# Optimization experiments

Hardware: AMD Instinct MI355X
Metric: run time of the kernel (lower is better)

Reference implementation:

```python
import jax, jax.numpy as jnp
import numpy as np

N_NODES = 100000

def gcn_conv(x, W, b, src, dst, n):
    # PyG GCNConv: h = x @ W; add self-loops; norm = D^-1/2 (A+I) D^-1/2; aggregate at dst.
    h = x @ W  # [N, out]
    deg = jnp.zeros((n,), h.dtype).at[dst].add(1.0) + 1.0  # +1 for self-loop
    d = jax.lax.rsqrt(deg)  # deg >= 1 always
    norm = d[src] * d[dst]  # [E]
    agg = jnp.zeros_like(h).at[dst].add(norm[:, None] * h[src])  # scatter-add neighbor messages
    agg = agg + h * (d * d)[:, None]  # self-loop contribution (norm = d_i^2)
    return agg + b


def setup_inputs() -> dict:
    key = jax.random.key(0)
    k1, k2, k3, k4 = jax.random.split(key, 4)
    F_in, H, C = 128, 64, 16
    E = 3200000
    x = jax.random.normal(k1, (N_NODES, F_in), dtype=jnp.float32)
    edges = jax.random.randint(k2, (E, 2), 0, N_NODES, dtype=jnp.int64)
    # Glorot-style init for weights, zero bias (as in GCNConv.reset_parameters)
    W1 = jax.random.normal(k3, (F_in, H), dtype=jnp.float32) * (1.0 / np.sqrt(F_in))
    b1 = jnp.zeros((H,), jnp.float32)
    W2 = jax.random.normal(k4, (H, C), dtype=jnp.float32) * (1.0 / np.sqrt(H))
    b2 = jnp.zeros((C,), jnp.float32)
    return {"x": x, "edges": edges, "W1": W1, "b1": b1, "W2": W2, "b2": b2}


def reference(x, edges, W1, b1, W2, b2):
    src, dst = edges[:, 0], edges[:, 1]
    h = jax.nn.relu(gcn_conv(x, W1, b1, src, dst, N_NODES))
    out = gcn_conv(h, W2, b2, src, dst, N_NODES)
    return out
```

## Files before the change

### kernel.cpp

```cpp
#include <hip/hip_runtime.h>

#define N_NODES 100000
#define F_IN    128
#define H_DIM   64
#define C_DIM   16
#define NBKT    391
#define CHUNK   8192
#define CAP     8960
#define MAXCH   400

typedef __attribute__((ext_vector_type(8))) short bf16x8;
typedef __attribute__((ext_vector_type(4))) float f32x4;

__device__ __forceinline__ unsigned bfr(float f) {
    unsigned u = __float_as_uint(f);
    return (u + (((u >> 16) & 1u) + 0x7FFFu)) >> 16;
}
__device__ __forceinline__ void accb(float4& a, uint2 u) {
    a.x += __uint_as_float(u.x << 16);
    a.y += __uint_as_float(u.x & 0xFFFF0000u);
    a.z += __uint_as_float(u.y << 16);
    a.w += __uint_as_float(u.y & 0xFFFF0000u);
}

__global__ __launch_bounds__(512) void k_bfill(const int2* __restrict__ edges,
                                               int* __restrict__ pairs_flat,
                                               int* __restrict__ cnts_g,
                                               int* __restrict__ lbase_g, int E) {
    __shared__ int2 sp[CHUNK];
    __shared__ int  cnt[NBKT];
    __shared__ int  lbase[NBKT];
    __shared__ int  scn[512];
    int t = threadIdx.x;
    for (int i = t; i < NBKT; i += 512) cnt[i] = 0;
    __syncthreads();
    int base = blockIdx.x * CHUNK;
    int m    = min(E - base, CHUNK);
    int2 ed[16];
    int  rk[16];
    #pragma unroll
    for (int i = 0; i < 16; ++i) {
        int e = i * 512 + t;
        if (e < m) {
            ed[i] = edges[base + e];
            rk[i] = atomicAdd(&cnt[ed[i].y >> 8], 1);
        }
    }
    __syncthreads();
    scn[t] = (t < NBKT) ? cnt[t] : 0;
    __syncthreads();
    #pragma unroll
    for (int off = 1; off < 512; off <<= 1) {
        int v = (t >= off) ? scn[t - off] : 0;
        __syncthreads();
        scn[t] += v;
        __syncthreads();
    }
    for (int b = t; b < NBKT; b += 512) {
        int c = cnt[b];
        int lb = scn[b] - c;
        lbase[b] = lb;
        cnts_g [blockIdx.x * NBKT + b] = c;
        lbase_g[blockIdx.x * NBKT + b] = lb;
    }
    __syncthreads();
    #pragma unroll
    for (int i = 0; i < 16; ++i) {
        int e = i * 512 + t;
        if (e < m) sp[lbase[ed[i].y >> 8] + rk[i]] = ed[i];
    }
    __syncthreads();
    #pragma unroll
    for (int i = 0; i < 16; ++i) {
        int idx = i * 512 + t;
        if (idx < m) {
            int2 p = sp[idx];
            pairs_flat[base + idx] = (p.x << 8) | (p.y & 255);
        }
    }
}

__global__ __launch_bounds__(1024) void k_bnode(const int* __restrict__ pairs_flat,
                                                const int* __restrict__ cnts_g,
                                                const int* __restrict__ lbase_g,
                                                int* __restrict__ csr_src,
                                                int* __restrict__ node_base,
                                                int* __restrict__ node_cnt,
                                                float* __restrict__ dinv, int nch) {
    __shared__ int spairs[CAP];
    __shared__ int sc[CAP];
    __shared__ int rcnt[MAXCH];
    __shared__ int rlb[MAXCH];
    __shared__ int roff[MAXCH];
    __shared__ int scn[512];
    __shared__ int cnt[256];
    __shared__ int row[256];
    __shared__ int wsum[4];
    __shared__ int mtot;
    int b = blockIdx.x;
    int t = threadIdx.x;
    if (t < 256) cnt[t] = 0;
    for (int i = t; i < nch; i += 1024) {
        rcnt[i] = cnts_g [i * NBKT + b];
        rlb[i]  = lbase_g[i * NBKT + b];
    }
    __syncthreads();
    if (t < 512) scn[t] = (t < nch) ? rcnt[t] : 0;
    __syncthreads();
    #pragma unroll
    for (int off = 1; off < 512; off <<= 1) {
        int v = 0;
        if (t < 512 && t >= off) v = scn[t - off];
        __syncthreads();
        if (t < 512) scn[t] += v;
        __syncthreads();
    }
    if (t < nch) roff[t] = scn[t] - rcnt[t];
    if (t == 0) mtot = scn[nch - 1];
    __syncthreads();
    int m = min(mtot, CAP);
    int grp = t >> 4, l16 = t & 15;
    for (int r = grp; r < nch; r += 64) {
        int c  = rcnt[r];
        int ro = roff[r];
        int rb = r * CHUNK + rlb[r];
        for (int j = l16; j < c; j += 16) {
            int pos = ro + j;
            if (pos < CAP) {
                int p  = pairs_flat[rb + j];
                int rk = atomicAdd(&cnt[p & 255], 1);
                spairs[pos] = p | (rk << 25);
            }
        }
    }
    __syncthreads();
    if (t < 256) {
        int c = cnt[t];
        int lane = t & 63, wv = t >> 6;
        int v = c;
        #pragma unroll
        for (int off = 1; off < 64; off <<= 1) {
            int u = __shfl_up(v, off);
            if (lane >= off) v += u;
        }
        if (lane == 63) wsum[wv] = v;
        __syncthreads();
        int woff = 0;
        #pragma unroll
        for (int w = 0; w < 4; ++w) woff += (w < wv) ? wsum[w] : 0;
        int incl = v + woff;
        row[t] = incl - c;
        int node = b * 256 + t;
        if (node < N_NODES) {
            node_base[node] = b * CAP + incl - c;
            node_cnt[node]  = c;
            dinv[node]      = rsqrtf((float)(c + 1));
        }
    } else {
        __syncthreads();
    }
    __syncthreads();
    for (int e = t; e < m; e += 1024) {
        int p = spairs[e];
        sc[row[p & 255] + ((unsigned)p >> 25)] = (p >> 8) & 0x1FFFF;
    }
    __syncthreads();
    for (int e = t; e < m; e += 1024)
        csr_src[b * CAP + e] = sc[e];
}

__global__ __launch_bounds__(256) void k_gemm1(const float* __restrict__ x,
                                               const float* __restrict__ W1,
                                               const float* __restrict__ dinv,
                                               uint2* __restrict__ g1b) {
    __shared__ short wt[64][132];
    int tid = threadIdx.x;
    {
        int n  = tid & 63;
        int k0 = (tid >> 6) * 32;
        #pragma unroll 8
        for (int k = 0; k < 32; ++k)
            wt[n][k0 + k] = (short)bfr(W1[(size_t)(k0 + k) * H_DIM + n]);
    }
    __syncthreads();

    int wave = tid >> 6, lane = tid & 63;
    int tile = blockIdx.x * 4 + wave;
    bool valid = tile < N_NODES / 16;
    int row0 = (valid ? tile : 0) * 16;
    int l15  = lane & 15;
    int kg   = lane >> 4;
    const float* xrow = x + (size_t)(row0 + l15) * F_IN;

    f32x4 ac0 = {0.f,0.f,0.f,0.f}, ac1 = ac0, ac2 = ac0, ac3 = ac0;
    #pragma unroll
    for (int ks = 0; ks < 4; ++ks) {
        int kb = ks * 32 + kg * 8;
        float4 p0 = *(const float4*)(xrow + kb);
        float4 p1 = *(const float4*)(xrow + kb + 4);
        bf16x8 a;
        a[0] = (short)bfr(p0.x); a[1] = (short)bfr(p0.y);
        a[2] = (short)bfr(p0.z); a[3] = (short)bfr(p0.w);
        a[4] = (short)bfr(p1.x); a[5] = (short)bfr(p1.y);
        a[6] = (short)bfr(p1.z); a[7] = (short)bfr(p1.w);
        bf16x8 b0 = *(const bf16x8*)&wt[l15     ][kb];
        bf16x8 b1 = *(const bf16x8*)&wt[l15 + 16][kb];
        bf16x8 b2 = *(const bf16x8*)&wt[l15 + 32][kb];
        bf16x8 b3 = *(const bf16x8*)&wt[l15 + 48][kb];
        ac0 = __builtin_amdgcn_mfma_f32_16x16x32_bf16(a, b0, ac0, 0, 0, 0);
        ac1 = __builtin_amdgcn_mfma_f32_16x16x32_bf16(a, b1, ac1, 0, 0, 0);
        ac2 = __builtin_amdgcn_mfma_f32_16x16x32_bf16(a, b2, ac2, 0, 0, 0);
        ac3 = __builtin_amdgcn_mfma_f32_16x16x32_bf16(a, b3, ac3, 0, 0, 0);
    }
    if (!valid) return;

    int rbase = row0 + kg * 4;
    #pragma unroll
    for (int r = 0; r < 4; ++r) {
        float di = dinv[rbase + r];
        size_t gro = (size_t)(rbase + r) * 16;
        #pragma unroll
        for (int ct = 0; ct < 4; ++ct) {
            float v = ((ct == 0) ? ac0[r] : (ct == 1) ? ac1[r] :
                       (ct == 2) ? ac2[r] : ac3[r]) * di;
            float v1 = __shfl_down(v, 1);
            float v2 = __shfl_down(v, 2);
            float v3 = __shfl_down(v, 3);
            if ((l15 & 3) == 0) {
                uint2 pk;
                pk.x = bfr(v)  | (bfr(v1) << 16);
                pk.y = bfr(v2) | (bfr(v3) << 16);
                g1b[gro + ct * 4 + (l15 >> 2)] = pk;
            }
        }
    }
}

__global__ __launch_bounds__(256) void k_gather1(const int* __restrict__ csr_src,
                                                 const int* __restrict__ base,
                                                 const int* __restrict__ cnt,
                                                 const float* __restrict__ dinv,
                                                 const uint2* __restrict__ g1b,
                                                 const float* __restrict__ b1,
                                                 const float* __restrict__ W2,
                                                 uint2* __restrict__ g2b) {
    __shared__ float  w2t[16 * 68];
    __shared__ float4 ysh[4][68];
    int tid = threadIdx.x;
    #pragma unroll
    for (int i = 0; i < 4; ++i) {
        int idx = i * 256 + tid;
        w2t[(idx & 15) * 68 + (idx >> 4)] = W2[idx];
    }
    __syncthreads();

    int lane = tid & 63;
    int wv   = tid >> 6;
    int grp  = lane >> 4;
    int l16  = lane & 15;
    int g0   = lane & 48;
    int node = ((blockIdx.x * 256 + tid) >> 6) * 4 + grp;
    int   b  = base[node];
    int   c  = cnt[node];
    float di = dinv[node];
    float4 acc = {0.f, 0.f, 0.f, 0.f};
    accb(acc, g1b[(size_t)node * 16 + l16]);

    for (int k0 = 0; k0 < c; k0 += 16) {
        int k = k0 + l16;
        int sidx = (k < c) ? csr_src[b + k] : 0;
        int nj = min(16, c - k0);
        int j = 0;
        for (; j + 4 <= nj; j += 4) {
            int s0 = __shfl(sidx, g0 + j + 0);
            int s1 = __shfl(sidx, g0 + j + 1);
            int s2 = __shfl(sidx, g0 + j + 2);
            int s3 = __shfl(sidx, g0 + j + 3);
            uint2 u0 = g1b[(size_t)s0 * 16 + l16];
            uint2 u1 = g1b[(size_t)s1 * 16 + l16];
            uint2 u2 = g1b[(size_t)s2 * 16 + l16];
            uint2 u3 = g1b[(size_t)s3 * 16 + l16];
            accb(acc, u0); accb(acc, u1); accb(acc, u2); accb(acc, u3);
        }
        for (; j < nj; ++j) {
            accb(acc, g1b[(size_t)__shfl(sidx, g0 + j) * 16 + l16]);
        }
    }

    float4 bv = ((const float4*)b1)[l16];
    float4 y;
    y.x = fmaxf(fmaf(di, acc.x, bv.x), 0.f) * di;
    y.y = fmaxf(fmaf(di, acc.y, bv.y), 0.f) * di;
    y.z = fmaxf(fmaf(di, acc.z, bv.z), 0.f) * di;
    y.w = fmaxf(fmaf(di, acc.w, bv.w), 0.f) * di;
    ysh[wv][grp * 17 + l16] = y;

    float o = 0.f;
    #pragma unroll
    for (int f4 = 0; f4 < 16; ++f4) {
        float4 yv = ysh[wv][grp * 17 + f4];
        const float4* wr = (const float4*)&w2t[l16 * 68 + f4 * 4];
        float4 wv4 = *wr;
        o = fmaf(yv.x, wv4.x, o);
        o = fmaf(yv.y, wv4.y, o);
        o = fmaf(yv.z, wv4.z, o);
        o = fmaf(yv.w, wv4.w, o);
    }
    float o1 = __shfl_down(o, 1);
    float o2 = __shfl_down(o, 2);
    float o3 = __shfl_down(o, 3);
    if ((l16 & 3) == 0) {
        uint2 pk;
        pk.x = bfr(o)  | (bfr(o1) << 16);
        pk.y = bfr(o2) | (bfr(o3) << 16);
        g2b[(size_t)node * 4 + (l16 >> 2)] = pk;
    }
}

__global__ __launch_bounds__(256) void k_gather2(const int* __restrict__ csr_src,
                                                 const int* __restrict__ base,
                                                 const int* __restrict__ cnt,
                                                 const float* __restrict__ dinv,
                                                 const uint2* __restrict__ g2b,
                                                 const float* __restrict__ b2,
                                                 float* __restrict__ out) {
    int tid  = threadIdx.x;
    int lane = tid & 63;
    int grp  = lane >> 2;
    int l4   = lane & 3;
    int g0   = lane & 60;
    int node = ((blockIdx.x * 256 + tid) >> 6) * 16 + grp;
    if (node >= N_NODES) return;
    int   b  = base[node];
    int   c  = cnt[node];
    float di = dinv[node];
    float4 acc = {0.f, 0.f, 0.f, 0.f};
    accb(acc, g2b[(size_t)node * 4 + l4]);

    for (int k0 = 0; k0 < c; k0 += 4) {
        int k = k0 + l4;
        int sidx = (k < c) ? csr_src[b + k] : 0;
        int nj = min(4, c - k0);
        if (nj == 4) {
            int s0 = __shfl(sidx, g0 + 0);
            int s1 = __shfl(sidx, g0 + 1);
            int s2 = __shfl(sidx, g0 + 2);
            int s3 = __shfl(sidx, g0 + 3);
            uint2 u0 = g2b[(size_t)s0 * 4 + l4];
            uint2 u1 = g2b[(size_t)s1 * 4 + l4];
            uint2 u2 = g2b[(size_t)s2 * 4 + l4];
            uint2 u3 = g2b[(size_t)s3 * 4 + l4];
            accb(acc, u0); accb(acc, u1); accb(acc, u2); accb(acc, u3);
        } else {
            for (int j = 0; j < nj; ++j)
                accb(acc, g2b[(size_t)__shfl(sidx, g0 + j) * 4 + l4]);
        }
    }
    float4 bv = ((const float4*)b2)[l4];
    float4 r  = { fmaf(di, acc.x, bv.x), fmaf(di, acc.y, bv.y),
                  fmaf(di, acc.z, bv.z), fmaf(di, acc.w, bv.w) };
    ((float4*)out)[(size_t)node * 4 + l4] = r;
}

extern "C" void kernel_launch(void* const* d_in, const int* in_sizes, int n_in,
                              void* d_out, int out_size, void* d_ws, size_t ws_size,
                              hipStream_t stream) {
    const float* x     = (const float*)d_in[0];
    const int*   edges = (const int*)d_in[1];
    const float* W1    = (const float*)d_in[2];
    const float* b1    = (const float*)d_in[3];
    const float* W2    = (const float*)d_in[4];
    const float* b2    = (const float*)d_in[5];
    float*       out   = (float*)d_out;

    const int E   = in_sizes[1] / 2;
    const int nch = (E + CHUNK - 1) / CHUNK;

    int*   pairs_flat = (int*)d_ws;
    uint2* g1b     = (uint2*)d_ws;
    uint2* g2b     = (uint2*)((float*)d_ws + (size_t)NBKT * CAP);
    int*   csr_src = (int*)g2b + (size_t)N_NODES * 8 + 64;
    int*   nbase   = csr_src + (size_t)NBKT * CAP;
    int*   ncnt    = nbase + N_NODES;
    float* dinv    = (float*)(ncnt + N_NODES);
    int*   cnts_g  = (int*)(dinv + N_NODES);
    int*   lbase_g = cnts_g + (size_t)nch * NBKT;

    k_bfill <<<nch, 512, 0, stream>>>((const int2*)edges, pairs_flat,
                                      cnts_g, lbase_g, E);
    k_bnode <<<NBKT, 1024, 0, stream>>>(pairs_flat, cnts_g, lbase_g, csr_src,
                                        nbase, ncnt, dinv, nch);

    k_gemm1   <<<(N_NODES / 16 + 3) / 4, 256, 0, stream>>>(x, W1, dinv, g1b);

    k_gather1 <<<6250, 256, 0, stream>>>(csr_src, nbase, ncnt, dinv, g1b, b1, W2, g2b);

    k_gather2 <<<1563, 256, 0, stream>>>(csr_src, nbase, ncnt, dinv, g2b, b2, out);
}
```

Baseline: 138.7 us.

## Fuse CSR node build with GEMM1 in one horizontally-split kernel

Merges the per-bucket CSR construction kernel and the first dense GEMM into a single launch, where the first 391 blocks build the CSR and the remaining blocks compute x@W1 independently. Because GEMM1 no longer has dinv available, the source-side normalization moves into the first gather, which now loads dinv per neighbor and applies it with an FMA. The CSR build is also changed from a rank-encoded two-phase scatter to a count pass followed by atomic position reservation, which reads pairs_flat twice. The workspace is re-laid out so g1b no longer aliases pairs_flat. The trade-off is an extra dinv gather per edge and a second pass over the pairs, in exchange for one fewer launch and overlapping the GEMM with the CSR build.

Result: no change. 138.6 us, median of 2 (-0.1%).

```diff
diff --git a/kernel.cpp b/kernel.cpp
--- a/kernel.cpp
+++ b/kernel.cpp
@@ -5,6 +5,7 @@
 #define H_DIM   64
 #define C_DIM   16
 #define NBKT    391
+#define NTILE   6250
 #define CHUNK   8192
 #define CAP     8960
 #define MAXCH   400
@@ -15,6 +16,12 @@
 __device__ __forceinline__ unsigned bfr(float f) {
     unsigned u = __float_as_uint(f);
     return (u + (((u >> 16) & 1u) + 0x7FFFu)) >> 16;
+}
+__device__ __forceinline__ void accbs(float4& a, uint2 u, float d) {
+    a.x = fmaf(d, __uint_as_float(u.x << 16),         a.x);
+    a.y = fmaf(d, __uint_as_float(u.x & 0xFFFF0000u), a.y);
+    a.z = fmaf(d, __uint_as_float(u.y << 16),         a.z);
+    a.w = fmaf(d, __uint_as_float(u.y & 0xFFFF0000u), a.w);
 }
 __device__ __forceinline__ void accb(float4& a, uint2 u) {
     a.x += __uint_as_float(u.x << 16);
@@ -80,157 +87,147 @@
     }
 }
 
-__global__ __launch_bounds__(1024) void k_bnode(const int* __restrict__ pairs_flat,
-                                                const int* __restrict__ cnts_g,
-                                                const int* __restrict__ lbase_g,
-                                                int* __restrict__ csr_src,
-                                                int* __restrict__ node_base,
-                                                int* __restrict__ node_cnt,
-                                                float* __restrict__ dinv, int nch) {
-    __shared__ int spairs[CAP];
-    __shared__ int sc[CAP];
-    __shared__ int rcnt[MAXCH];
-    __shared__ int rlb[MAXCH];
-    __shared__ int roff[MAXCH];
-    __shared__ int scn[512];
-    __shared__ int cnt[256];
-    __shared__ int row[256];
-    __shared__ int wsum[4];
-    __shared__ int mtot;
-    int b = blockIdx.x;
+struct SmemU {
+    union {
+        struct {
+            int sc[CAP];
+            int rcnt[MAXCH];
+            int rlb[MAXCH];
+            int cnt[256];
+            int row[256];
+            int wsum[4];
+            int mtot;
+        } b;
+        short wt[64][132];
+    };
+};
+
+__global__ __launch_bounds__(1024) void k_fat(const int* __restrict__ pairs_flat,
+                                              const int* __restrict__ cnts_g,
+                                              const int* __restrict__ lbase_g,
+                                              int* __restrict__ csr_src,
+                                              int* __restrict__ node_base,
+                                              int* __restrict__ node_cnt,
+                                              float* __restrict__ dinv, int nch,
+                                              const float* __restrict__ x,
+                                              const float* __restrict__ W1,
+                                              uint2* __restrict__ g1b) {
+    __shared__ SmemU sm;
     int t = threadIdx.x;
-    if (t < 256) cnt[t] = 0;
-    for (int i = t; i < nch; i += 1024) {
-        rcnt[i] = cnts_g [i * NBKT + b];
-        rlb[i]  = lbase_g[i * NBKT + b];
-    }
-    __syncthreads();
-    if (t < 512) scn[t] = (t < nch) ? rcnt[t] : 0;
-    __syncthreads();
-    #pragma unroll
-    for (int off = 1; off < 512; off <<= 1) {
-        int v = 0;
-        if (t < 512 && t >= off) v = scn[t - off];
-        __syncthreads();
-        if (t < 512) scn[t] += v;
-        __syncthreads();
-    }
-    if (t < nch) roff[t] = scn[t] - rcnt[t];
-    if (t == 0) mtot = scn[nch - 1];
-    __syncthreads();
-    int m = min(mtot, CAP);
-    int grp = t >> 4, l16 = t & 15;
-    for (int r = grp; r < nch; r += 64) {
-        int c  = rcnt[r];
-        int ro = roff[r];
-        int rb = r * CHUNK + rlb[r];
-        for (int j = l16; j < c; j += 16) {
-            int pos = ro + j;
-            if (pos < CAP) {
-                int p  = pairs_flat[rb + j];
-                int rk = atomicAdd(&cnt[p & 255], 1);
-                spairs[pos] = p | (rk << 25);
+
+    if (blockIdx.x < NBKT) {
+        int b = blockIdx.x;
+        int lane = t & 63, wv = t >> 6;
+        if (t < 256) sm.b.cnt[t] = 0;
+        for (int i = t; i < nch; i += 1024) {
+            sm.b.rcnt[i] = cnts_g [i * NBKT + b];
+            sm.b.rlb[i]  = lbase_g[i * NBKT + b];
+        }
+        __syncthreads();
+        int grp = t >> 4, l16 = t & 15;
+        for (int r = grp; r < nch; r += 64) {
+            int c  = sm.b.rcnt[r];
+            int rb = r * CHUNK + sm.b.rlb[r];
+            for (int j = l16; j < c; j += 16)
+                atomicAdd(&sm.b.cnt[pairs_flat[rb + j] & 255], 1);
+        }
+        __syncthreads();
+        if (t < 256) {
+            int c = sm.b.cnt[t];
+            int v = c;
+            #pragma unroll
+            for (int off = 1; off < 64; off <<= 1) {
+                int u = __shfl_up(v, off);
+                if (lane >= off) v += u;
             }
-        }
-    }
-    __syncthreads();
-    if (t < 256) {
-        int c = cnt[t];
-        int lane = t & 63, wv = t >> 6;
-        int v = c;
+            if (lane == 63) sm.b.wsum[wv] = v;
+            __syncthreads();
+            int woff = 0;
+            #pragma unroll
+            for (int w = 0; w < 4; ++w) woff += (w < wv) ? sm.b.wsum[w] : 0;
+            int incl = v + woff;
+            sm.b.row[t] = incl - c;
+            if (t == 255) sm.b.mtot = incl;
+            int node = b * 256 + t;
+            if (node < N_NODES) {
+                node_base[node] = b * CAP + incl - c;
+                node_cnt[node]  = c;
+                dinv[node]      = rsqrtf((float)(c + 1));
+            }
+        } else {
+            __syncthreads();
+        }
+        __syncthreads();
+        int m = min(sm.b.mtot, CAP);
+        for (int r = grp; r < nch; r += 64) {
+            int c  = sm.b.rcnt[r];
+            int rb = r * CHUNK + sm.b.rlb[r];
+            for (int j = l16; j < c; j += 16) {
+                int p   = pairs_flat[rb + j];
+                int pos = atomicAdd(&sm.b.row[p & 255], 1);
+                if (pos < CAP) sm.b.sc[pos] = (p >> 8) & 0x1FFFF;
+            }
+        }
+        __syncthreads();
+        for (int e = t; e < m; e += 1024)
+            csr_src[b * CAP + e] = sm.b.sc[e];
+    } else {
+        {
+            int n  = t & 63;
+            int k0 = (t >> 6) * 8;
+            #pragma unroll
+            for (int k = 0; k < 8; ++k)
+                sm.wt[n][k0 + k] = (short)bfr(W1[(size_t)(k0 + k) * H_DIM + n]);
+        }
+        __syncthreads();
+
+        int wave = t >> 6, lane = t & 63;
+        int tile = (blockIdx.x - NBKT) * 16 + wave;
+        bool valid = tile < NTILE;
+        int row0 = (valid ? tile : 0) * 16;
+        int l15  = lane & 15;
+        int kg   = lane >> 4;
+        const float* xrow = x + (size_t)(row0 + l15) * F_IN;
+
+        f32x4 ac0 = {0.f,0.f,0.f,0.f}, ac1 = ac0, ac2 = ac0, ac3 = ac0;
         #pragma unroll
-        for (int off = 1; off < 64; off <<= 1) {
-            int u = __shfl_up(v, off);
-            if (lane >= off) v += u;
-        }
-        if (lane == 63) wsum[wv] = v;
-        __syncthreads();
-        int woff = 0;
+        for (int ks = 0; ks < 4; ++ks) {
+            int kb = ks * 32 + kg * 8;
+            float4 p0 = *(const float4*)(xrow + kb);
+            float4 p1 = *(const float4*)(xrow + kb + 4);
+            bf16x8 a;
+            a[0] = (short)bfr(p0.x); a[1] = (short)bfr(p0.y);
+            a[2] = (short)bfr(p0.z); a[3] = (short)bfr(p0.w);
+            a[4] = (short)bfr(p1.x); a[5] = (short)bfr(p1.y);
+            a[6] = (short)bfr(p1.z); a[7] = (short)bfr(p1.w);
+            bf16x8 b0 = *(const bf16x8*)&sm.wt[l15     ][kb];
+            bf16x8 b1 = *(const bf16x8*)&sm.wt[l15 + 16][kb];
+            bf16x8 b2 = *(const bf16x8*)&sm.wt[l15 + 32][kb];
+            bf16x8 b3 = *(const bf16x8*)&sm.wt[l15 + 48][kb];
+            ac0 = __builtin_amdgcn_mfma_f32_16x16x32_bf16(a, b0, ac0, 0, 0, 0);
+            ac1 = __builtin_amdgcn_mfma_f32_16x16x32_bf16(a, b1, ac1, 0, 0, 0);
+            ac2 = __builtin_amdgcn_mfma_f32_16x16x32_bf16(a, b2, ac2, 0, 0, 0);
+            ac3 = __builtin_amdgcn_mfma_f32_16x16x32_bf16(a, b3, ac3, 0, 0, 0);
+        }
+        if (!valid) return;
+
+        int rbase = row0 + kg * 4;
         #pragma unroll
-        for (int w = 0; w < 4; ++w) woff += (w < wv) ? wsum[w] : 0;
-        int incl = v + woff;
-        row[t] = incl - c;
-        int node = b * 256 + t;
-        if (node < N_NODES) {
-            node_base[node] = b * CAP + incl - c;
-            node_cnt[node]  = c;
-            dinv[node]      = rsqrtf((float)(c + 1));
-        }
-    } else {
-        __syncthreads();
-    }
-    __syncthreads();
-    for (int e = t; e < m; e += 1024) {
-        int p = spairs[e];
-        sc[row[p & 255] + ((unsigned)p >> 25)] = (p >> 8) & 0x1FFFF;
-    }
-    __syncthreads();
-    for (int e = t; e < m; e += 1024)
-        csr_src[b * CAP + e] = sc[e];
-}
-
-__global__ __launch_bounds__(256) void k_gemm1(const float* __restrict__ x,
-                                               const float* __restrict__ W1,
-                                               const float* __restrict__ dinv,
-                                               uint2* __restrict__ g1b) {
-    __shared__ short wt[64][132];
-    int tid = threadIdx.x;
-    {
-        int n  = tid & 63;
-        int k0 = (tid >> 6) * 32;
-        #pragma unroll 8
-        for (int k = 0; k < 32; ++k)
-            wt[n][k0 + k] = (short)bfr(W1[(size_t)(k0 + k) * H_DIM + n]);
-    }
-    __syncthreads();
-
-    int wave = tid >> 6, lane = tid & 63;
-    int tile = blockIdx.x * 4 + wave;
-    bool valid = tile < N_NODES / 16;
-    int row0 = (valid ? tile : 0) * 16;
-    int l15  = lane & 15;
-    int kg   = lane >> 4;
-    const float* xrow = x + (size_t)(row0 + l15) * F_IN;
-
-    f32x4 ac0 = {0.f,0.f,0.f,0.f}, ac1 = ac0, ac2 = ac0, ac3 = ac0;
-    #pragma unroll
-    for (int ks = 0; ks < 4; ++ks) {
-        int kb = ks * 32 + kg * 8;
-        float4 p0 = *(const float4*)(xrow + kb);
-        float4 p1 = *(const float4*)(xrow + kb + 4);
-        bf16x8 a;
-        a[0] = (short)bfr(p0.x); a[1] = (short)bfr(p0.y);
-        a[2] = (short)bfr(p0.z); a[3] = (short)bfr(p0.w);
-        a[4] = (short)bfr(p1.x); a[5] = (short)bfr(p1.y);
-        a[6] = (short)bfr(p1.z); a[7] = (short)bfr(p1.w);
-        bf16x8 b0 = *(const bf16x8*)&wt[l15     ][kb];
-        bf16x8 b1 = *(const bf16x8*)&wt[l15 + 16][kb];
-        bf16x8 b2 = *(const bf16x8*)&wt[l15 + 32][kb];
-        bf16x8 b3 = *(const bf16x8*)&wt[l15 + 48][kb];
-        ac0 = __builtin_amdgcn_mfma_f32_16x16x32_bf16(a, b0, ac0, 0, 0, 0);
-        ac1 = __builtin_amdgcn_mfma_f32_16x16x32_bf16(a, b1, ac1, 0, 0, 0);
-        ac2 = __builtin_amdgcn_mfma_f32_16x16x32_bf16(a, b2, ac2, 0, 0, 0);
-        ac3 = __builtin_amdgcn_mfma_f32_16x16x32_bf16(a, b3, ac3, 0, 0, 0);
-    }
-    if (!valid) return;
-
-    int rbase = row0 + kg * 4;
-    #pragma unroll
-    for (int r = 0; r < 4; ++r) {
-        float di = dinv[rbase + r];
-        size_t gro = (size_t)(rbase + r) * 16;
-        #pragma unroll
-        for (int ct = 0; ct < 4; ++ct) {
-            float v = ((ct == 0) ? ac0[r] : (ct == 1) ? ac1[r] :
-                       (ct == 2) ? ac2[r] : ac3[r]) * di;
-            float v1 = __shfl_down(v, 1);
-            float v2 = __shfl_down(v, 2);
-            float v3 = __shfl_down(v, 3);
-            if ((l15 & 3) == 0) {
-                uint2 pk;
-                pk.x = bfr(v)  | (bfr(v1) << 16);
-                pk.y = bfr(v2) | (bfr(v3) << 16);
-                g1b[gro + ct * 4 + (l15 >> 2)] = pk;
+        for (int r = 0; r < 4; ++r) {
+            size_t gro = (size_t)(rbase + r) * 16;
+            #pragma unroll
+            for (int ct = 0; ct < 4; ++ct) {
+                float v = (ct == 0) ? ac0[r] : (ct == 1) ? ac1[r] :
+                          (ct == 2) ? ac2[r] : ac3[r];
+                float v1 = __shfl_down(v, 1);
+                float v2 = __shfl_down(v, 2);
+                float v3 = __shfl_down(v, 3);
+                if ((l15 & 3) == 0) {
+                    uint2 pk;
+                    pk.x = bfr(v)  | (bfr(v1) << 16);
+                    pk.y = bfr(v2) | (bfr(v3) << 16);
+                    g1b[gro + ct * 4 + (l15 >> 2)] = pk;
+                }
             }
         }
     }
@@ -264,26 +261,34 @@
     int   c  = cnt[node];
     float di = dinv[node];
     float4 acc = {0.f, 0.f, 0.f, 0.f};
-    accb(acc, g1b[(size_t)node * 16 + l16]);
+    accbs(acc, g1b[(size_t)node * 16 + l16], di);
 
     for (int k0 = 0; k0 < c; k0 += 16) {
         int k = k0 + l16;
-        int sidx = (k < c) ? csr_src[b + k] : 0;
+        int   sidx = 0;
+        float dn   = 0.f;
+        if (k < c) { sidx = csr_src[b + k]; dn = dinv[sidx]; }
         int nj = min(16, c - k0);
         int j = 0;
         for (; j + 4 <= nj; j += 4) {
-            int s0 = __shfl(sidx, g0 + j + 0);
-            int s1 = __shfl(sidx, g0 + j + 1);
-            int s2 = __shfl(sidx, g0 + j + 2);
-            int s3 = __shfl(sidx, g0 + j + 3);
+            int   s0 = __shfl(sidx, g0 + j + 0);
+            int   s1 = __shfl(sidx, g0 + j + 1);
+            int   s2 = __shfl(sidx, g0 + j + 2);
+            int   s3 = __shfl(sidx, g0 + j + 3);
+            float d0 = __shfl(dn,   g0 + j + 0);
+            float d1 = __shfl(dn,   g0 + j + 1);
+            float d2 = __shfl(dn,   g0 + j + 2);
+            float d3 = __shfl(dn,   g0 + j + 3);
             uint2 u0 = g1b[(size_t)s0 * 16 + l16];
             uint2 u1 = g1b[(size_t)s1 * 16 + l16];
             uint2 u2 = g1b[(size_t)s2 * 16 + l16];
             uint2 u3 = g1b[(size_t)s3 * 16 + l16];
-            accb(acc, u0); accb(acc, u1); accb(acc, u2); accb(acc, u3);
+            accbs(acc, u0, d0); accbs(acc, u1, d1);
+            accbs(acc, u2, d2); accbs(acc, u3, d3);
         }
         for (; j < nj; ++j) {
-            accb(acc, g1b[(size_t)__shfl(sidx, g0 + j) * 16 + l16]);
+            accbs(acc, g1b[(size_t)__shfl(sidx, g0 + j) * 16 + l16],
+                  __shfl(dn, g0 + j));
         }
     }
 
@@ -377,8 +382,8 @@
     const int nch = (E + CHUNK - 1) / CHUNK;
 
     int*   pairs_flat = (int*)d_ws;
-    uint2* g1b     = (uint2*)d_ws;
-    uint2* g2b     = (uint2*)((float*)d_ws + (size_t)NBKT * CAP);
+    uint2* g1b     = (uint2*)(pairs_flat + (size_t)nch * CHUNK);
+    uint2* g2b     = (uint2*)((int*)g1b + (size_t)N_NODES * 32);
     int*   csr_src = (int*)g2b + (size_t)N_NODES * 8 + 64;
     int*   nbase   = csr_src + (size_t)NBKT * CAP;
     int*   ncnt    = nbase + N_NODES;
@@ -388,10 +393,9 @@
 
     k_bfill <<<nch, 512, 0, stream>>>((const int2*)edges, pairs_flat,
                                       cnts_g, lbase_g, E);
-    k_bnode <<<NBKT, 1024, 0, stream>>>(pairs_flat, cnts_g, lbase_g, csr_src,
-                                        nbase, ncnt, dinv, nch);
-
-    k_gemm1   <<<(N_NODES / 16 + 3) / 4, 256, 0, stream>>>(x, W1, dinv, g1b);
+
+    k_fat <<<NBKT + 391, 1024, 0, stream>>>(pairs_flat, cnts_g, lbase_g, csr_src,
+                                            nbase, ncnt, dinv, nch, x, W1, g1b);
 
     k_gather1 <<<6250, 256, 0, stream>>>(csr_src, nbase, ncnt, dinv, g1b, b1, W2, g2b);
 
```
